# Kernel tuning notes

Hardware: AMD Instinct MI355X
Metric: run time of the kernel (lower is better)

The kernel has to match this reference:

```python
import jax, jax.numpy as jnp
import numpy as np

N_NODES = 300000   # cell instances
N_NETS  = 200000   # hyperedges (nets); each net has exactly one source/driver
E_SINK  = 1000000  # sink (node->net) pin edges
NODE_DIM, NET_DIM, EMB = 32, 16, 64
L, NUM_VN = 3, 1000
OUT_NODE, OUT_NET = 4, 4
SLOPE = 0.01  # torch leaky_relu default negative_slope


def leaky(x):
    return jnp.where(x >= 0, x, SLOPE * x)


def _lin(key, fan_in, fan_out):
    kw, kb = jax.random.split(key)
    b = 1.0 / np.sqrt(fan_in)
    W = jax.random.uniform(kw, (fan_in, fan_out), jnp.float32, -b, b)
    bb = jax.random.uniform(kb, (fan_out,), jnp.float32, -b, b)
    return W, bb


def setup_inputs() -> dict:
    key = jax.random.key(0)
    ks = iter(jax.random.split(key, 64))
    d = {}
    d["node_features"] = jax.random.normal(next(ks), (N_NODES, NODE_DIM), jnp.float32)
    d["net_features"] = jax.random.normal(next(ks), (N_NETS, NET_DIM), jnp.float32)
    d["src_nodes"] = jax.random.randint(next(ks), (N_NETS,), 0, N_NODES)   # driver node of net i
    d["sink_nodes"] = jax.random.randint(next(ks), (E_SINK,), 0, N_NODES)
    d["sink_nets"] = jax.random.randint(next(ks), (E_SINK,), 0, N_NETS)
    d["edge_weight"] = jax.random.uniform(next(ks), (E_SINK,), jnp.float32)
    d["batch"] = jax.random.randint(next(ks), (N_NODES,), 0, NUM_VN)       # node -> virtual node id
    # node / net encoders
    d["ne_W1"], d["ne_b1"] = _lin(next(ks), NODE_DIM, 2 * EMB)
    d["ne_W2"], d["ne_b2"] = _lin(next(ks), 2 * EMB, EMB)
    d["te_W1"], d["te_b1"] = _lin(next(ks), NET_DIM, EMB)
    d["te_W2"], d["te_b2"] = _lin(next(ks), EMB, EMB)
    d["vn_emb"] = jnp.zeros((EMB,), jnp.float32)  # torch: init.constant_(weight, 0)
    # HyperConv layers, stacked over L
    Wnet, bnet, Wnode, bnode = [], [], [], []
    for _ in range(L):
        W, b = _lin(next(ks), 3 * EMB, EMB); Wnet.append(W); bnet.append(b)
        W, b = _lin(next(ks), 2 * EMB, EMB); Wnode.append(W); bnode.append(b)
    d["conv_Wnet"] = jnp.stack(Wnet); d["conv_bnet"] = jnp.stack(bnet)
    d["conv_Wnode"] = jnp.stack(Wnode); d["conv_bnode"] = jnp.stack(bnode)
    # virtual-node MLPs (L-1 of them)
    vW1, vb1, vW2, vb2 = [], [], [], []
    for _ in range(L - 1):
        W, b = _lin(next(ks), EMB, EMB); vW1.append(W); vb1.append(b)
        W, b = _lin(next(ks), EMB, EMB); vW2.append(W); vb2.append(b)
    d["vn_W1"] = jnp.stack(vW1); d["vn_b1"] = jnp.stack(vb1)
    d["vn_W2"] = jnp.stack(vW2); d["vn_b2"] = jnp.stack(vb2)
    # output heads
    d["fc1n_W"], d["fc1n_b"] = _lin(next(ks), EMB, 256)
    d["fc2n_W"], d["fc2n_b"] = _lin(next(ks), 256, OUT_NODE)
    d["fc1e_W"], d["fc1e_b"] = _lin(next(ks), EMB, 64)
    d["fc2e_W"], d["fc2e_b"] = _lin(next(ks), 64, OUT_NET)
    return d


def _forward(node_features, net_features, edge_weight,
             ne_W1, ne_b1, ne_W2, ne_b2, te_W1, te_b1, te_W2, te_b2,
             vn_emb, conv_Wnet, conv_bnet, conv_Wnode, conv_bnode,
             vn_W1, vn_b1, vn_W2, vn_b2,
             fc1n_W, fc1n_b, fc2n_W, fc2n_b, fc1e_W, fc1e_b, fc2e_W, fc2e_b,
             src_nodes, sink_nodes, sink_nets, batch):
    h = leaky(node_features @ ne_W1 + ne_b1) @ ne_W2 + ne_b2   # [N, EMB]
    g = leaky(net_features @ te_W1 + te_b1) @ te_W2 + te_b2    # [M, EMB]
    w = edge_weight[:, None]
    vn = jnp.broadcast_to(vn_emb, (NUM_VN, EMB))               # embedding of all-zero indices
    for l in range(L):
        h = h + vn[batch]
        # node -> net (hyperedge) aggregation: driver message + weighted sink sum
        agg_src = h[src_nodes]                                             # [M, EMB]
        agg_sink = jax.ops.segment_sum(h[sink_nodes] * w, sink_nets, num_segments=N_NETS)
        g = jnp.concatenate([g, agg_src, agg_sink], axis=-1) @ conv_Wnet[l] + conv_bnet[l]
        # net -> node aggregation
        back = jax.ops.segment_sum(g, src_nodes, num_segments=N_NODES) \
             + jax.ops.segment_sum(g[sink_nets] * w, sink_nodes, num_segments=N_NODES)
        h = jnp.concatenate([h, back], axis=-1) @ conv_Wnode[l] + conv_bnode[l]
        h = leaky(h)
        g = leaky(g)
        if l < L - 1:
            pooled = jax.ops.segment_max(h, batch, num_segments=NUM_VN)   # global_max_pool
            tmp = pooled + vn
            vn = vn + (leaky(tmp @ vn_W1[l] + vn_b1[l]) @ vn_W2[l] + vn_b2[l])
    node_rep = jnp.abs(leaky(h @ fc1n_W + fc1n_b) @ fc2n_W + fc2n_b)
    net_rep = jnp.abs(leaky(g @ fc1e_W + fc1e_b) @ fc2e_W + fc2e_b)
    return node_rep, net_rep


def reference(node_features, net_features, edge_weight,
              ne_W1, ne_b1, ne_W2, ne_b2, te_W1, te_b1, te_W2, te_b2,
              vn_emb, conv_Wnet, conv_bnet, conv_Wnode, conv_bnode,
              vn_W1, vn_b1, vn_W2, vn_b2,
              fc1n_W, fc1n_b, fc2n_W, fc2n_b, fc1e_W, fc1e_b, fc2e_W, fc2e_b,
              src_nodes, sink_nodes, sink_nets, batch):
    return _forward(node_features, net_features, edge_weight,
                    ne_W1, ne_b1, ne_W2, ne_b2, te_W1, te_b1, te_W2, te_b2,
                    vn_emb, conv_Wnet, conv_bnet, conv_Wnode, conv_bnode,
                    vn_W1, vn_b1, vn_W2, vn_b2,
                    fc1n_W, fc1n_b, fc2n_W, fc2n_b, fc1e_W, fc1e_b, fc2e_W, fc2e_b,
                    src_nodes, sink_nodes, sink_nets, batch)
```

## Files before the change

kernel.cpp:

```cpp
#include <hip/hip_runtime.h>
#include <cstdint>

static constexpr int N_NODES = 300000;
static constexpr int N_NETS  = 200000;
static constexpr int E_SINK  = 1000000;
static constexpr int NODE_DIM = 32;
static constexpr int NET_DIM  = 16;
static constexpr int EMB = 64;
static constexpr int NUM_VN = 1000;
#define SLOPE 0.01f

typedef __attribute__((ext_vector_type(8))) short bhalf8;
typedef __attribute__((ext_vector_type(4))) float floatx4;
typedef unsigned short u16;

__device__ __forceinline__ float leaky(float x) { return x >= 0.f ? x : SLOPE * x; }

__device__ __forceinline__ unsigned bf16_rne(float x) {
    unsigned u = __float_as_uint(x);
    return (u + 0x7FFFu + ((u >> 16) & 1u)) >> 16;
}
__device__ __forceinline__ void split1(float x, u16& hh, u16& ll) {
    unsigned hb = bf16_rne(x);
    float fh = __uint_as_float(hb << 16);
    unsigned lb = bf16_rne(x - fh);
    hh = (u16)hb; ll = (u16)lb;
}
__device__ __forceinline__ void split8v(const float* x, bhalf8& ah, bhalf8& al) {
#pragma unroll
    for (int e = 0; e < 8; ++e) {
        u16 hh, ll; split1(x[e], hh, ll);
        ah[e] = (short)hh; al[e] = (short)ll;
    }
}
__device__ __forceinline__ float rec1(short h, short l) {
    return __uint_as_float(((unsigned)(u16)h) << 16) +
           __uint_as_float(((unsigned)(u16)l) << 16);
}

__device__ __forceinline__ void afrag_f32(const float* rowp, int kbase, bhalf8& ah, bhalf8& al) {
    float4 v0 = *(const float4*)(rowp + kbase);
    float4 v1 = *(const float4*)(rowp + kbase + 4);
    float x[8] = {v0.x, v0.y, v0.z, v0.w, v1.x, v1.y, v1.z, v1.w};
    split8v(x, ah, al);
}
__device__ __forceinline__ void afrag_hl(const u16* hi, const u16* lo, size_t off,
                                         bhalf8& ah, bhalf8& al) {
    ah = *(const bhalf8*)(hi + off);
    al = *(const bhalf8*)(lo + off);
}

__device__ __forceinline__ floatx4 mm3(bhalf8 ah, bhalf8 al, bhalf8 wh, bhalf8 wl, floatx4 c) {
    c = __builtin_amdgcn_mfma_f32_16x16x32_bf16(ah, wh, c, 0, 0, 0);
    c = __builtin_amdgcn_mfma_f32_16x16x32_bf16(ah, wl, c, 0, 0, 0);
    c = __builtin_amdgcn_mfma_f32_16x16x32_bf16(al, wh, c, 0, 0, 0);
    return c;
}

static constexpr int OFF_NEW1 = 0;
static constexpr int OFF_NEW2 = 4096;
static constexpr int OFF_TEW1 = 12288;
static constexpr int OFF_TEW2 = 14336;
static constexpr int OFF_CWNET = 18432;
static constexpr int OFF_CWNODE = 55296;
static constexpr int OFF_FC1N = 79872;
static constexpr int OFF_FC1E = 96256;
static constexpr int W_TOTAL  = 100352;

__global__ void k_prep_w(const float* __restrict__ neW1, const float* __restrict__ neW2,
                         const float* __restrict__ teW1, const float* __restrict__ teW2,
                         const float* __restrict__ cWnet, const float* __restrict__ cWnode,
                         const float* __restrict__ fc1n, const float* __restrict__ fc1e,
                         u16* __restrict__ wfh, u16* __restrict__ wfl)
{
    int i = blockIdx.x * 256 + threadIdx.x;
    if (i >= W_TOTAL) return;
    int r, ncols, K; const float* src;
    if (i < OFF_NEW2)        { r = i;             src = neW1;  ncols = 128; K = 32; }
    else if (i < OFF_TEW1)   { r = i - OFF_NEW2;  src = neW2;  ncols = 64;  K = 128; }
    else if (i < OFF_TEW2)   { r = i - OFF_TEW1;  src = teW1;  ncols = 64;  K = 16; }
    else if (i < OFF_CWNET)  { r = i - OFF_TEW2;  src = teW2;  ncols = 64;  K = 64; }
    else if (i < OFF_CWNODE) { int t = i - OFF_CWNET;  int l = t / 12288; r = t % 12288;
                               src = cWnet + (size_t)l * 192 * 64; ncols = 64; K = 192; }
    else if (i < OFF_FC1N)   { int t = i - OFF_CWNODE; int l = t / 8192;  r = t % 8192;
                               src = cWnode + (size_t)l * 128 * 64; ncols = 64; K = 128; }
    else if (i < OFF_FC1E)   { r = i - OFF_FC1N;  src = fc1n;  ncols = 256; K = 64; }
    else                     { r = i - OFF_FC1E;  src = fc1e;  ncols = 64;  K = 64; }
    int e = r & 7, g = (r >> 3) & 3;
    int cidx = r >> 5;
    int col = cidx % ncols, kt = cidx / ncols;
    int k = kt * 32 + g * 8 + e;
    float v = (k < K) ? src[(size_t)k * ncols + col] : 0.f;
    u16 hh, ll; split1(v, hh, ll);
    wfh[i] = hh; wfl[i] = ll;
}

__device__ __forceinline__ bhalf8 ldw(const u16* p, int idx) {
    return *(const bhalf8*)(p + idx);
}

__global__ void k_hist_edges(const int* __restrict__ sink_nets, const int* __restrict__ sink_nodes,
                             int* __restrict__ cnt_net, int* __restrict__ cnt_node)
{
    int e = blockIdx.x * 256 + threadIdx.x;
    if (e >= E_SINK) return;
    atomicAdd(&cnt_net[sink_nets[e]], 1);
    atomicAdd(&cnt_node[sink_nodes[e]], 1);
}

__global__ void k_hist_misc(const int* __restrict__ src_nodes, const int* __restrict__ batch,
                            int* __restrict__ cnt_src, int* __restrict__ cnt_vn)
{
    int i = blockIdx.x * 256 + threadIdx.x;
    if (i < N_NETS) atomicAdd(&cnt_src[src_nodes[i]], 1);
    if (i < N_NODES) atomicAdd(&cnt_vn[batch[i]], 1);
}

__global__ void k_scan1(const int* __restrict__ cnt, int n, int* __restrict__ bsum) {
    __shared__ int s[256];
    int i = blockIdx.x * 256 + threadIdx.x;
    s[threadIdx.x] = (i < n) ? cnt[i] : 0;
    __syncthreads();
    for (int off = 128; off; off >>= 1) {
        if (threadIdx.x < off) s[threadIdx.x] += s[threadIdx.x + off];
        __syncthreads();
    }
    if (threadIdx.x == 0) bsum[blockIdx.x] = s[0];
}

__global__ void k_scan2(int* __restrict__ data, int n) {
    __shared__ int s[256];
    __shared__ int carry_s;
    int tid = threadIdx.x;
    if (tid == 0) carry_s = 0;
    __syncthreads();
    for (int base = 0; base < n; base += 256) {
        int i = base + tid;
        int v = (i < n) ? data[i] : 0;
        s[tid] = v;
        __syncthreads();
        for (int off = 1; off < 256; off <<= 1) {
            int t = (tid >= off) ? s[tid - off] : 0;
            __syncthreads();
            s[tid] += t;
            __syncthreads();
        }
        int excl = s[tid] - v + carry_s;
        if (i < n) data[i] = excl;
        __syncthreads();
        if (tid == 255) carry_s = excl + v;
        __syncthreads();
    }
}

__global__ void k_scan3(const int* __restrict__ cnt, int n, const int* __restrict__ bsum,
                        int* __restrict__ start) {
    __shared__ int s[256];
    int i = blockIdx.x * 256 + threadIdx.x;
    int v = (i < n) ? cnt[i] : 0;
    s[threadIdx.x] = v;
    __syncthreads();
    for (int off = 1; off < 256; off <<= 1) {
        int t = (threadIdx.x >= off) ? s[threadIdx.x - off] : 0;
        __syncthreads();
        s[threadIdx.x] += t;
        __syncthreads();
    }
    int excl = s[threadIdx.x] - v + bsum[blockIdx.x];
    if (i < n) start[i] = excl;
    if (i == n - 1) start[n] = excl + v;
}

__global__ void k_fill_edges(const int* __restrict__ sink_nets, const int* __restrict__ sink_nodes,
                             const float* __restrict__ ew,
                             const int* __restrict__ net_start, const int* __restrict__ node_start,
                             int* __restrict__ cur_net, int* __restrict__ cur_node,
                             int* __restrict__ e_node, float* __restrict__ e_w,
                             int* __restrict__ e2_net, float* __restrict__ e2_w)
{
    int e = blockIdx.x * 256 + threadIdx.x;
    if (e >= E_SINK) return;
    int tn = sink_nets[e], dn = sink_nodes[e];
    float w = ew[e];
    int p = net_start[tn] + atomicAdd(&cur_net[tn], 1);
    e_node[p] = dn; e_w[p] = w;
    int q = node_start[dn] + atomicAdd(&cur_node[dn], 1);
    e2_net[q] = tn; e2_w[q] = w;
}

__global__ void k_fill_misc(const int* __restrict__ src_nodes, const int* __restrict__ batch,
                            const int* __restrict__ src_start, const int* __restrict__ vn_start,
                            int* __restrict__ cur_src, int* __restrict__ cur_vn,
                            int* __restrict__ s_net, int* __restrict__ b_node)
{
    int i = blockIdx.x * 256 + threadIdx.x;
    if (i < N_NETS) {
        int d = src_nodes[i];
        int p = src_start[d] + atomicAdd(&cur_src[d], 1);
        s_net[p] = i;
    }
    if (i < N_NODES) {
        int v = batch[i];
        int p = vn_start[v] + atomicAdd(&cur_vn[v], 1);
        b_node[p] = i;
    }
}

__global__ __launch_bounds__(256) void k_gather_agg(
    u16* __restrict__ agg_hi, u16* __restrict__ agg_lo,
    const u16* __restrict__ h_hi, const u16* __restrict__ h_lo,
    const int* __restrict__ net_start, const int* __restrict__ e_node, const float* __restrict__ e_w)
{
    int w = (blockIdx.x * 256 + threadIdx.x) >> 6;
    if (w >= N_NETS) return;
    int lane = threadIdx.x & 63;
    int grp = lane >> 3, l8 = lane & 7;
    int j0 = net_start[w], j1 = net_start[w + 1];
    float a[8] = {0.f, 0.f, 0.f, 0.f, 0.f, 0.f, 0.f, 0.f};
    for (int j = j0 + grp; j < j1; j += 8) {
        int idx = e_node[j];
        float wt = e_w[j];
        size_t off = (size_t)idx * 64 + l8 * 8;
        bhalf8 vh = *(const bhalf8*)(h_hi + off);
        bhalf8 vl = *(const bhalf8*)(h_lo + off);
#pragma unroll
        for (int e = 0; e < 8; ++e) a[e] += wt * rec1(vh[e], vl[e]);
    }
#pragma unroll
    for (int e = 0; e < 8; ++e) {
        a[e] += __shfl_xor(a[e], 8, 64);
        a[e] += __shfl_xor(a[e], 16, 64);
        a[e] += __shfl_xor(a[e], 32, 64);
    }
    if (grp == 0) {
        bhalf8 oh, ol;
        split8v(a, oh, ol);
        size_t off = (size_t)w * 64 + l8 * 8;
        *(bhalf8*)(agg_hi + off) = oh;
        *(bhalf8*)(agg_lo + off) = ol;
    }
}

__global__ __launch_bounds__(256) void k_gather_back(
    u16* __restrict__ back_hi, u16* __restrict__ back_lo,
    const u16* __restrict__ g_hi, const u16* __restrict__ g_lo,
    const int* __restrict__ src_start, const int* __restrict__ s_net,
    const int* __restrict__ node_start, const int* __restrict__ e2_net, const float* __restrict__ e2_w)
{
    int w = (blockIdx.x * 256 + threadIdx.x) >> 6;
    if (w >= N_NODES) return;
    int lane = threadIdx.x & 63;
    int grp = lane >> 3, l8 = lane & 7;
    float a[8] = {0.f, 0.f, 0.f, 0.f, 0.f, 0.f, 0.f, 0.f};
    int j0 = src_start[w], j1 = src_start[w + 1];
    for (int j = j0 + grp; j < j1; j += 8) {
        int idx = s_net[j];
        size_t off = (size_t)idx * 64 + l8 * 8;
        bhalf8 vh = *(const bhalf8*)(g_hi + off);
        bhalf8 vl = *(const bhalf8*)(g_lo + off);
#pragma unroll
        for (int e = 0; e < 8; ++e) {
            float f = rec1(vh[e], vl[e]);
            a[e] += (f >= 0.f) ? f : f * 100.f;
        }
    }
    j0 = node_start[w]; j1 = node_start[w + 1];
    for (int j = j0 + grp; j < j1; j += 8) {
        int idx = e2_net[j];
        float wt = e2_w[j];
        size_t off = (size_t)idx * 64 + l8 * 8;
        bhalf8 vh = *(const bhalf8*)(g_hi + off);
        bhalf8 vl = *(const bhalf8*)(g_lo + off);
#pragma unroll
        for (int e = 0; e < 8; ++e) {
            float f = rec1(vh[e], vl[e]);
            a[e] += wt * ((f >= 0.f) ? f : f * 100.f);
        }
    }
#pragma unroll
    for (int e = 0; e < 8; ++e) {
        a[e] += __shfl_xor(a[e], 8, 64);
        a[e] += __shfl_xor(a[e], 16, 64);
        a[e] += __shfl_xor(a[e], 32, 64);
    }
    if (grp == 0) {
        bhalf8 oh, ol;
        split8v(a, oh, ol);
        size_t off = (size_t)w * 64 + l8 * 8;
        *(bhalf8*)(back_hi + off) = oh;
        *(bhalf8*)(back_lo + off) = ol;
    }
}

__global__ __launch_bounds__(256) void k_pool_gather(
    float* __restrict__ pooled, const u16* __restrict__ h_hi, const u16* __restrict__ h_lo,
    const int* __restrict__ vn_start, const int* __restrict__ b_node)
{
    __shared__ float red[32][64];
    int tid = threadIdx.x;
    int grp = tid >> 3, l8 = tid & 7;
    int v = blockIdx.x;
    int j0 = vn_start[v], j1 = vn_start[v + 1];
    const float NEG = -__builtin_inff();
    float m[8] = {NEG, NEG, NEG, NEG, NEG, NEG, NEG, NEG};
    for (int j = j0 + grp; j < j1; j += 32) {
        int nd = b_node[j];
        size_t off = (size_t)nd * 64 + l8 * 8;
        bhalf8 vh = *(const bhalf8*)(h_hi + off);
        bhalf8 vl = *(const bhalf8*)(h_lo + off);
#pragma unroll
        for (int e = 0; e < 8; ++e) m[e] = fmaxf(m[e], rec1(vh[e], vl[e]));
    }
#pragma unroll
    for (int e = 0; e < 8; ++e) red[grp][l8 * 8 + e] = m[e];
    __syncthreads();
    if (tid < 64) {
        float mm = red[0][tid];
#pragma unroll
        for (int q = 1; q < 32; ++q) mm = fmaxf(mm, red[q][tid]);
        pooled[(size_t)v * 64 + tid] = mm;
    }
}

__global__ __launch_bounds__(256) void k_node_enc(
    const float* __restrict__ x, const u16* __restrict__ wfh, const u16* __restrict__ wfl,
    const float* __restrict__ b1, const float* __restrict__ b2,
    u16* __restrict__ h_hi, u16* __restrict__ h_lo)
{
    __shared__ u16 t_hi[64][136];
    __shared__ u16 t_lo[64][136];
    int lane = threadIdx.x & 63, wid = threadIdx.x >> 6;
    int g16 = lane >> 4, l15 = lane & 15;
    int rbase = blockIdx.x * 64;

    bhalf8 W1H[2], W1L[2];
#pragma unroll
    for (int s = 0; s < 2; ++s) {
        int col = wid * 16 + s * 64 + l15;
        int fo = OFF_NEW1 + (col * 4 + g16) * 8;
        W1H[s] = ldw(wfh, fo); W1L[s] = ldw(wfl, fo);
    }
    bhalf8 W2H[4], W2L[4];
    int cs = wid * 16 + l15;
#pragma unroll
    for (int kt = 0; kt < 4; ++kt) {
        int fo = OFF_NEW2 + ((kt * 64 + cs) * 4 + g16) * 8;
        W2H[kt] = ldw(wfh, fo); W2L[kt] = ldw(wfl, fo);
    }

#pragma unroll
    for (int ms = 0; ms < 4; ++ms) {
        int r = min(rbase + ms * 16 + l15, N_NODES - 1);
        bhalf8 ah, al;
        afrag_f32(x + (size_t)r * NODE_DIM, g16 * 8, ah, al);
#pragma unroll
        for (int s = 0; s < 2; ++s) {
            floatx4 acc = {0.f, 0.f, 0.f, 0.f};
            acc = mm3(ah, al, W1H[s], W1L[s], acc);
            int hc = wid * 16 + s * 64 + l15;
            float bb = b1[hc];
#pragma unroll
            for (int i = 0; i < 4; ++i) {
                u16 hh, ll;
                split1(leaky(acc[i] + bb), hh, ll);
                t_hi[ms * 16 + g16 * 4 + i][hc] = hh;
                t_lo[ms * 16 + g16 * 4 + i][hc] = ll;
            }
        }
    }
    __syncthreads();

    float bias = b2[cs];
#pragma unroll
    for (int ms = 0; ms < 4; ++ms) {
        floatx4 acc = {0.f, 0.f, 0.f, 0.f};
#pragma unroll
        for (int kt = 0; kt < 4; ++kt) {
            bhalf8 ah = *(const bhalf8*)(&t_hi[ms * 16 + l15][kt * 32 + g16 * 8]);
            bhalf8 al = *(const bhalf8*)(&t_lo[ms * 16 + l15][kt * 32 + g16 * 8]);
            acc = mm3(ah, al, W2H[kt], W2L[kt], acc);
        }
#pragma unroll
        for (int i = 0; i < 4; ++i) {
            int r = rbase + ms * 16 + g16 * 4 + i;
            if (r < N_NODES) {
                u16 hh, ll;
                split1(acc[i] + bias, hh, ll);
                h_hi[(size_t)r * 64 + cs] = hh;
                h_lo[(size_t)r * 64 + cs] = ll;
            }
        }
    }
}

__global__ __launch_bounds__(256) void k_net_enc(
    const float* __restrict__ x, const u16* __restrict__ wfh, const u16* __restrict__ wfl,
    const float* __restrict__ b1, const float* __restrict__ b2,
    u16* __restrict__ g_hi, u16* __restrict__ g_lo)
{
    __shared__ u16 t_hi[64][72];
    __shared__ u16 t_lo[64][72];
    int lane = threadIdx.x & 63, wid = threadIdx.x >> 6;
    int g16 = lane >> 4, l15 = lane & 15;
    int rbase = blockIdx.x * 64;
    int cs = wid * 16 + l15;

    int fo = OFF_TEW1 + (cs * 4 + g16) * 8;
    bhalf8 W1H = ldw(wfh, fo), W1L = ldw(wfl, fo);
    bhalf8 W2H[2], W2L[2];
#pragma unroll
    for (int kt = 0; kt < 2; ++kt) {
        int f2 = OFF_TEW2 + ((kt * 64 + cs) * 4 + g16) * 8;
        W2H[kt] = ldw(wfh, f2); W2L[kt] = ldw(wfl, f2);
    }

#pragma unroll
    for (int ms = 0; ms < 4; ++ms) {
        int r = min(rbase + ms * 16 + l15, N_NETS - 1);
        bhalf8 ah = {0,0,0,0,0,0,0,0}, al = {0,0,0,0,0,0,0,0};
        if (g16 < 2) afrag_f32(x + (size_t)r * NET_DIM, g16 * 8, ah, al);
        floatx4 acc = {0.f, 0.f, 0.f, 0.f};
        acc = mm3(ah, al, W1H, W1L, acc);
        float bb = b1[cs];
#pragma unroll
        for (int i = 0; i < 4; ++i) {
            u16 hh, ll;
            split1(leaky(acc[i] + bb), hh, ll);
            t_hi[ms * 16 + g16 * 4 + i][cs] = hh;
            t_lo[ms * 16 + g16 * 4 + i][cs] = ll;
        }
    }
    __syncthreads();

    float bias = b2[cs];
#pragma unroll
    for (int ms = 0; ms < 4; ++ms) {
        floatx4 acc = {0.f, 0.f, 0.f, 0.f};
#pragma unroll
        for (int kt = 0; kt < 2; ++kt) {
            bhalf8 ah = *(const bhalf8*)(&t_hi[ms * 16 + l15][kt * 32 + g16 * 8]);
            bhalf8 al = *(const bhalf8*)(&t_lo[ms * 16 + l15][kt * 32 + g16 * 8]);
            acc = mm3(ah, al, W2H[kt], W2L[kt], acc);
        }
#pragma unroll
        for (int i = 0; i < 4; ++i) {
            int r = rbase + ms * 16 + g16 * 4 + i;
            if (r < N_NETS) {
                u16 hh, ll;
                split1(acc[i] + bias, hh, ll);
                g_hi[(size_t)r * 64 + cs] = hh;
                g_lo[(size_t)r * 64 + cs] = ll;
            }
        }
    }
}

__global__ void k_vn_init(float* __restrict__ vn, const float* __restrict__ vn_emb) {
    int idx = blockIdx.x * blockDim.x + threadIdx.x;
    if (idx < NUM_VN * EMB) vn[idx] = vn_emb[idx & 63];
}

__global__ void k_add_vn(u16* __restrict__ h_hi, u16* __restrict__ h_lo,
                         const float* __restrict__ vn, const int* __restrict__ batch) {
    int idx = blockIdx.x * blockDim.x + threadIdx.x;
    if (idx >= N_NODES * 8) return;
    int n = idx >> 3, c8 = idx & 7;
    size_t off = (size_t)n * 64 + c8 * 8;
    bhalf8 vh = *(const bhalf8*)(h_hi + off);
    bhalf8 vl = *(const bhalf8*)(h_lo + off);
    const float* vr = vn + (size_t)batch[n] * 64 + c8 * 8;
    float out[8];
#pragma unroll
    for (int e = 0; e < 8; ++e) out[e] = rec1(vh[e], vl[e]) + vr[e];
    bhalf8 oh, ol;
    split8v(out, oh, ol);
    *(bhalf8*)(h_hi + off) = oh;
    *(bhalf8*)(h_lo + off) = ol;
}

__global__ __launch_bounds__(256) void k_conv_net(
    u16* g_hi, u16* g_lo,
    const u16* __restrict__ h_hi, const u16* __restrict__ h_lo,
    const u16* __restrict__ s_hi, const u16* __restrict__ s_lo,
    const int* __restrict__ src,
    const u16* __restrict__ wfh, const u16* __restrict__ wfl, int wbase,
    const float* __restrict__ b)
{
    int lane = threadIdx.x & 63, wid = threadIdx.x >> 6;
    int g16 = lane >> 4, l15 = lane & 15;
    int rbase = blockIdx.x * 64;
    int cs = wid * 16 + l15;

    bhalf8 WH[6], WL[6];
#pragma unroll
    for (int kt = 0; kt < 6; ++kt) {
        int fo = wbase + ((kt * 64 + cs) * 4 + g16) * 8;
        WH[kt] = ldw(wfh, fo); WL[kt] = ldw(wfl, fo);
    }

    bhalf8 GH[4][2], GL[4][2];
#pragma unroll
    for (int ms = 0; ms < 4; ++ms) {
        int r = min(rbase + ms * 16 + l15, N_NETS - 1);
#pragma unroll
        for (int kt = 0; kt < 2; ++kt)
            afrag_hl(g_hi, g_lo, (size_t)r * 64 + kt * 32 + g16 * 8, GH[ms][kt], GL[ms][kt]);
    }
    __syncthreads();

    float bias = b[cs];
#pragma unroll
    for (int ms = 0; ms < 4; ++ms) {
        floatx4 acc = {0.f, 0.f, 0.f, 0.f};
#pragma unroll
        for (int kt = 0; kt < 2; ++kt) acc = mm3(GH[ms][kt], GL[ms][kt], WH[kt], WL[kt], acc);
        int ar = min(rbase + ms * 16 + l15, N_NETS - 1);
        size_t srow = (size_t)src[ar] * 64;
#pragma unroll
        for (int kt = 0; kt < 2; ++kt) {
            bhalf8 ah, al;
            afrag_hl(h_hi, h_lo, srow + kt * 32 + g16 * 8, ah, al);
            acc = mm3(ah, al, WH[2 + kt], WL[2 + kt], acc);
        }
#pragma unroll
        for (int kt = 0; kt < 2; ++kt) {
            bhalf8 ah, al;
            afrag_hl(s_hi, s_lo, (size_t)ar * 64 + kt * 32 + g16 * 8, ah, al);
            acc = mm3(ah, al, WH[4 + kt], WL[4 + kt], acc);
        }
#pragma unroll
        for (int i = 0; i < 4; ++i) {
            int r = rbase + ms * 16 + g16 * 4 + i;
            if (r < N_NETS) {
                u16 hh, ll;
                split1(leaky(acc[i] + bias), hh, ll);
                g_hi[(size_t)r * 64 + cs] = hh;
                g_lo[(size_t)r * 64 + cs] = ll;
            }
        }
    }
}

__global__ __launch_bounds__(256) void k_conv_node(
    u16* h_hi, u16* h_lo,
    const u16* __restrict__ s_hi, const u16* __restrict__ s_lo,
    const u16* __restrict__ wfh, const u16* __restrict__ wfl, int wbase,
    const float* __restrict__ b)
{
    int lane = threadIdx.x & 63, wid = threadIdx.x >> 6;
    int g16 = lane >> 4, l15 = lane & 15;
    int rbase = blockIdx.x * 64;
    int cs = wid * 16 + l15;

    bhalf8 WH[4], WL[4];
#pragma unroll
    for (int kt = 0; kt < 4; ++kt) {
        int fo = wbase + ((kt * 64 + cs) * 4 + g16) * 8;
        WH[kt] = ldw(wfh, fo); WL[kt] = ldw(wfl, fo);
    }

    bhalf8 HH[4][2], HL[4][2];
#pragma unroll
    for (int ms = 0; ms < 4; ++ms) {
        int r = min(rbase + ms * 16 + l15, N_NODES - 1);
#pragma unroll
        for (int kt = 0; kt < 2; ++kt)
            afrag_hl(h_hi, h_lo, (size_t)r * 64 + kt * 32 + g16 * 8, HH[ms][kt], HL[ms][kt]);
    }
    __syncthreads();

    float bias = b[cs];
#pragma unroll
    for (int ms = 0; ms < 4; ++ms) {
        floatx4 acc = {0.f, 0.f, 0.f, 0.f};
#pragma unroll
        for (int kt = 0; kt < 2; ++kt) acc = mm3(HH[ms][kt], HL[ms][kt], WH[kt], WL[kt], acc);
        int ar = min(rbase + ms * 16 + l15, N_NODES - 1);
#pragma unroll
        for (int kt = 0; kt < 2; ++kt) {
            bhalf8 ah, al;
            afrag_hl(s_hi, s_lo, (size_t)ar * 64 + kt * 32 + g16 * 8, ah, al);
            acc = mm3(ah, al, WH[2 + kt], WL[2 + kt], acc);
        }
#pragma unroll
        for (int i = 0; i < 4; ++i) {
            int r = rbase + ms * 16 + g16 * 4 + i;
            if (r < N_NODES) {
                u16 hh, ll;
                split1(leaky(acc[i] + bias), hh, ll);
                h_hi[(size_t)r * 64 + cs] = hh;
                h_lo[(size_t)r * 64 + cs] = ll;
            }
        }
    }
}

__global__ __launch_bounds__(256) void k_vn_update(
    float* __restrict__ vn, const float* __restrict__ pooled,
    const float* __restrict__ W1, const float* __restrict__ b1,
    const float* __restrict__ W2, const float* __restrict__ b2)
{
    int wv = threadIdx.x >> 6, lane = threadIdx.x & 63;
    int v = blockIdx.x * 4 + wv;
    if (v >= NUM_VN) return;
    float p = pooled[(size_t)v * 64 + lane];
    float vv = vn[v * 64 + lane];
    float tmp = p + vv;
    float t1 = b1[lane];
#pragma unroll 16
    for (int k = 0; k < 64; ++k) t1 += __shfl(tmp, k, 64) * W1[k * 64 + lane];
    t1 = leaky(t1);
    float t2 = b2[lane];
#pragma unroll 16
    for (int k = 0; k < 64; ++k) t2 += __shfl(t1, k, 64) * W2[k * 64 + lane];
    vn[v * 64 + lane] = vv + t2;
}

__global__ __launch_bounds__(256) void k_fc_node(
    float* __restrict__ out, const u16* __restrict__ h_hi, const u16* __restrict__ h_lo,
    const u16* __restrict__ wfh, const u16* __restrict__ wfl,
    const float* __restrict__ b1, const float* __restrict__ W2, const float* __restrict__ b2)
{
    __shared__ float red[4][64][4];
    int lane = threadIdx.x & 63, wid = threadIdx.x >> 6;
    int g16 = lane >> 4, l15 = lane & 15;
    int rbase = blockIdx.x * 64;

    bhalf8 W1H[4][2], W1L[4][2];
    float4 w2v[4];
    float b1v[4];
#pragma unroll
    for (int s = 0; s < 4; ++s) {
        int hc = wid * 16 + s * 64 + l15;
#pragma unroll
        for (int kt = 0; kt < 2; ++kt) {
            int fo = OFF_FC1N + ((kt * 256 + hc) * 4 + g16) * 8;
            W1H[s][kt] = ldw(wfh, fo); W1L[s][kt] = ldw(wfl, fo);
        }
        w2v[s] = *(const float4*)(W2 + hc * 4);
        b1v[s] = b1[hc];
    }

#pragma unroll
    for (int ms = 0; ms < 4; ++ms) {
        int r = min(rbase + ms * 16 + l15, N_NODES - 1);
        bhalf8 ah[2], al[2];
#pragma unroll
        for (int kt = 0; kt < 2; ++kt)
            afrag_hl(h_hi, h_lo, (size_t)r * 64 + kt * 32 + g16 * 8, ah[kt], al[kt]);
        float po[4][4] = {{0.f,0.f,0.f,0.f},{0.f,0.f,0.f,0.f},{0.f,0.f,0.f,0.f},{0.f,0.f,0.f,0.f}};
#pragma unroll
        for (int s = 0; s < 4; ++s) {
            floatx4 acc = {0.f, 0.f, 0.f, 0.f};
#pragma unroll
            for (int kt = 0; kt < 2; ++kt) acc = mm3(ah[kt], al[kt], W1H[s][kt], W1L[s][kt], acc);
#pragma unroll
            for (int i = 0; i < 4; ++i) {
                float act = leaky(acc[i] + b1v[s]);
                po[i][0] += act * w2v[s].x;
                po[i][1] += act * w2v[s].y;
                po[i][2] += act * w2v[s].z;
                po[i][3] += act * w2v[s].w;
            }
        }
#pragma unroll
        for (int i = 0; i < 4; ++i)
#pragma unroll
            for (int o = 0; o < 4; ++o) {
                po[i][o] += __shfl_xor(po[i][o], 1, 64);
                po[i][o] += __shfl_xor(po[i][o], 2, 64);
                po[i][o] += __shfl_xor(po[i][o], 4, 64);
                po[i][o] += __shfl_xor(po[i][o], 8, 64);
            }
        if (l15 == 0) {
#pragma unroll
            for (int i = 0; i < 4; ++i)
#pragma unroll
                for (int o = 0; o < 4; ++o)
                    red[wid][ms * 16 + g16 * 4 + i][o] = po[i][o];
        }
    }
    __syncthreads();
    int tid = threadIdx.x;
    int row = tid >> 2, o = tid & 3;
    float sum = red[0][row][o] + red[1][row][o] + red[2][row][o] + red[3][row][o];
    int r = rbase + row;
    if (r < N_NODES) out[(size_t)r * 4 + o] = fabsf(sum + b2[o]);
}

__global__ __launch_bounds__(256) void k_fc_net(
    float* __restrict__ out, const u16* __restrict__ g_hi, const u16* __restrict__ g_lo,
    const u16* __restrict__ wfh, const u16* __restrict__ wfl,
    const float* __restrict__ b1, const float* __restrict__ W2, const float* __restrict__ b2)
{
    __shared__ float red[4][64][4];
    int lane = threadIdx.x & 63, wid = threadIdx.x >> 6;
    int g16 = lane >> 4, l15 = lane & 15;
    int rbase = blockIdx.x * 64;
    int cs = wid * 16 + l15;

    bhalf8 W1H[2], W1L[2];
#pragma unroll
    for (int kt = 0; kt < 2; ++kt) {
        int fo = OFF_FC1E + ((kt * 64 + cs) * 4 + g16) * 8;
        W1H[kt] = ldw(wfh, fo); W1L[kt] = ldw(wfl, fo);
    }
    float4 w2v = *(const float4*)(W2 + cs * 4);
    float b1v = b1[cs];

#pragma unroll
    for (int ms = 0; ms < 4; ++ms) {
        int r = min(rbase + ms * 16 + l15, N_NETS - 1);
        bhalf8 ah[2], al[2];
#pragma unroll
        for (int kt = 0; kt < 2; ++kt)
            afrag_hl(g_hi, g_lo, (size_t)r * 64 + kt * 32 + g16 * 8, ah[kt], al[kt]);
        floatx4 acc = {0.f, 0.f, 0.f, 0.f};
#pragma unroll
        for (int kt = 0; kt < 2; ++kt) acc = mm3(ah[kt], al[kt], W1H[kt], W1L[kt], acc);
        float po[4][4];
#pragma unroll
        for (int i = 0; i < 4; ++i) {
            float act = leaky(acc[i] + b1v);
            po[i][0] = act * w2v.x;
            po[i][1] = act * w2v.y;
            po[i][2] = act * w2v.z;
            po[i][3] = act * w2v.w;
        }
#pragma unroll
        for (int i = 0; i < 4; ++i)
#pragma unroll
            for (int o = 0; o < 4; ++o) {
                po[i][o] += __shfl_xor(po[i][o], 1, 64);
                po[i][o] += __shfl_xor(po[i][o], 2, 64);
                po[i][o] += __shfl_xor(po[i][o], 4, 64);
                po[i][o] += __shfl_xor(po[i][o], 8, 64);
            }
        if (l15 == 0) {
#pragma unroll
            for (int i = 0; i < 4; ++i)
#pragma unroll
                for (int o = 0; o < 4; ++o)
                    red[wid][ms * 16 + g16 * 4 + i][o] = po[i][o];
        }
    }
    __syncthreads();
    int tid = threadIdx.x;
    int row = tid >> 2, o = tid & 3;
    float sum = red[0][row][o] + red[1][row][o] + red[2][row][o] + red[3][row][o];
    int r = rbase + row;
    if (r < N_NETS) out[(size_t)r * 4 + o] = fabsf(sum + b2[o]);
}

extern "C" void kernel_launch(void* const* d_in, const int* in_sizes, int n_in,
                              void* d_out, int out_size, void* d_ws, size_t ws_size,
                              hipStream_t stream)
{
    const float* node_features = (const float*)d_in[0];
    const float* net_features  = (const float*)d_in[1];
    const int*   src_nodes     = (const int*)d_in[2];
    const int*   sink_nodes    = (const int*)d_in[3];
    const int*   sink_nets     = (const int*)d_in[4];
    const float* edge_weight   = (const float*)d_in[5];
    const int*   batch         = (const int*)d_in[6];
    const float* ne_W1 = (const float*)d_in[7];
    const float* ne_b1 = (const float*)d_in[8];
    const float* ne_W2 = (const float*)d_in[9];
    const float* ne_b2 = (const float*)d_in[10];
    const float* te_W1 = (const float*)d_in[11];
    const float* te_b1 = (const float*)d_in[12];
    const float* te_W2 = (const float*)d_in[13];
    const float* te_b2 = (const float*)d_in[14];
    const float* vn_emb = (const float*)d_in[15];
    const float* conv_Wnet  = (const float*)d_in[16];
    const float* conv_bnet  = (const float*)d_in[17];
    const float* conv_Wnode = (const float*)d_in[18];
    const float* conv_bnode = (const float*)d_in[19];
    const float* vn_W1 = (const float*)d_in[20];
    const float* vn_b1 = (const float*)d_in[21];
    const float* vn_W2 = (const float*)d_in[22];
    const float* vn_b2 = (const float*)d_in[23];
    const float* fc1n_W = (const float*)d_in[24];
    const float* fc1n_b = (const float*)d_in[25];
    const float* fc2n_W = (const float*)d_in[26];
    const float* fc2n_b = (const float*)d_in[27];
    const float* fc1e_W = (const float*)d_in[28];
    const float* fc1e_b = (const float*)d_in[29];
    const float* fc2e_W = (const float*)d_in[30];
    const float* fc2e_b = (const float*)d_in[31];

    float* out_node = (float*)d_out;
    float* out_net  = out_node + (size_t)N_NODES * 4;

    u16* h_hi = (u16*)d_ws;
    u16* h_lo = h_hi + (size_t)N_NODES * 64;
    u16* g_hi = h_lo + (size_t)N_NODES * 64;
    u16* g_lo = g_hi + (size_t)N_NETS * 64;
    u16* s_hi = g_lo + (size_t)N_NETS * 64;
    u16* s_lo = s_hi + (size_t)N_NODES * 64;
    u16* wfh  = s_lo + (size_t)N_NODES * 64;
    u16* wfl  = wfh + W_TOTAL;
    float* vn     = (float*)(wfl + W_TOTAL);
    float* pooled = vn + (size_t)NUM_VN * EMB;
    int* net_start  = (int*)(pooled + (size_t)NUM_VN * EMB);
    int* node_start = net_start + (N_NETS + 1);
    int* src_start  = node_start + (N_NODES + 1);
    int* vn_start   = src_start + (N_NODES + 1);
    int*   e_node = vn_start + (NUM_VN + 1);
    float* e_w    = (float*)(e_node + E_SINK);
    int*   e2_net = (int*)(e_w + E_SINK);
    float* e2_w   = (float*)(e2_net + E_SINK);
    int*   s_net  = (int*)(e2_w + E_SINK);
    int*   b_node = s_net + N_NETS;
    int*   cnt    = b_node + N_NODES;
    int*   cnt_net  = cnt;
    int*   cnt_node = cnt + N_NETS;
    int*   cnt_src  = cnt_node + N_NODES;
    int*   cnt_vn   = cnt_src + N_NODES;
    const int CNT_TOTAL = N_NETS + N_NODES + N_NODES + NUM_VN;
    int*   bsum   = cnt + CNT_TOTAL;

    const int nodeTiles = (N_NODES + 63) / 64;
    const int netTiles  = (N_NETS + 63) / 64;
    const int vnBlocks  = (NUM_VN + 3) / 4;
    const int vnElemBlocks  = (NUM_VN * EMB + 255) / 256;
    const int addVnBlocks  = (N_NODES * 8 + 255) / 256;
    const int edgeThreadBlocks = (E_SINK + 255) / 256;
    const int miscThreadBlocks = (N_NODES + 255) / 256;
    const int netWaveBlocks  = (N_NETS + 3) / 4;
    const int nodeWaveBlocks = (N_NODES + 3) / 4;
    const int prepBlocks = (W_TOTAL + 255) / 256;

    hipMemsetAsync(cnt, 0, (size_t)CNT_TOTAL * sizeof(int), stream);
    k_hist_edges<<<edgeThreadBlocks, 256, 0, stream>>>(sink_nets, sink_nodes, cnt_net, cnt_node);
    k_hist_misc<<<miscThreadBlocks, 256, 0, stream>>>(src_nodes, batch, cnt_src, cnt_vn);

    auto scan = [&](int* cnt_arr, int n, int* start_arr) {
        int nb = (n + 255) / 256;
        k_scan1<<<nb, 256, 0, stream>>>(cnt_arr, n, bsum);
        k_scan2<<<1, 256, 0, stream>>>(bsum, nb);
        k_scan3<<<nb, 256, 0, stream>>>(cnt_arr, n, bsum, start_arr);
    };
    scan(cnt_net, N_NETS, net_start);
    scan(cnt_node, N_NODES, node_start);
    scan(cnt_src, N_NODES, src_start);
    scan(cnt_vn, NUM_VN, vn_start);

    hipMemsetAsync(cnt, 0, (size_t)CNT_TOTAL * sizeof(int), stream);
    k_fill_edges<<<edgeThreadBlocks, 256, 0, stream>>>(sink_nets, sink_nodes, edge_weight,
        net_start, node_start, cnt_net, cnt_node, e_node, e_w, e2_net, e2_w);
    k_fill_misc<<<miscThreadBlocks, 256, 0, stream>>>(src_nodes, batch, src_start, vn_start,
        cnt_src, cnt_vn, s_net, b_node);

    k_prep_w<<<prepBlocks, 256, 0, stream>>>(ne_W1, ne_W2, te_W1, te_W2,
                                             conv_Wnet, conv_Wnode, fc1n_W, fc1e_W, wfh, wfl);
    k_node_enc<<<nodeTiles, 256, 0, stream>>>(node_features, wfh, wfl, ne_b1, ne_b2, h_hi, h_lo);
    k_net_enc<<<netTiles, 256, 0, stream>>>(net_features, wfh, wfl, te_b1, te_b2, g_hi, g_lo);
    k_vn_init<<<vnElemBlocks, 256, 0, stream>>>(vn, vn_emb);

    for (int l = 0; l < 3; ++l) {
        k_add_vn<<<addVnBlocks, 256, 0, stream>>>(h_hi, h_lo, vn, batch);

        k_gather_agg<<<netWaveBlocks, 256, 0, stream>>>(s_hi, s_lo, h_hi, h_lo,
                                                        net_start, e_node, e_w);
        k_conv_net<<<netTiles, 256, 0, stream>>>(g_hi, g_lo, h_hi, h_lo, s_hi, s_lo, src_nodes,
            wfh, wfl, OFF_CWNET + l * 12288, conv_bnet + (size_t)l * 64);

        k_gather_back<<<nodeWaveBlocks, 256, 0, stream>>>(s_hi, s_lo, g_hi, g_lo,
            src_start, s_net, node_start, e2_net, e2_w);
        k_conv_node<<<nodeTiles, 256, 0, stream>>>(h_hi, h_lo, s_hi, s_lo,
            wfh, wfl, OFF_CWNODE + l * 8192, conv_bnode + (size_t)l * 64);

        if (l < 2) {
            k_pool_gather<<<NUM_VN, 256, 0, stream>>>(pooled, h_hi, h_lo, vn_start, b_node);
            k_vn_update<<<vnBlocks, 256, 0, stream>>>(vn, pooled,
                vn_W1 + (size_t)l * 64 * 64, vn_b1 + (size_t)l * 64,
                vn_W2 + (size_t)l * 64 * 64, vn_b2 + (size_t)l * 64);
        }
    }

    k_fc_node<<<nodeTiles, 256, 0, stream>>>(out_node, h_hi, h_lo, wfh, wfl,
                                             fc1n_b, fc2n_W, fc2n_b);
    k_fc_net<<<netTiles, 256, 0, stream>>>(out_net, g_hi, g_lo, wfh, wfl,
                                           fc1e_b, fc2e_W, fc2e_b);
}
```

Before: 1.792 ms.

## Keep fp32 copies of node/net features for gathers and pack edge index+weight

Adds optional fp32 mirrors of h and of the raw pre-activation g, written by the encoder and conv epilogues, so the sparse gather, back-scatter and pooling kernels read one contiguous fp32 row instead of two bf16 hi/lo arrays and then reconstructing. The back gather reads raw g directly and skips undoing the leaky activation. Edge index and weight are packed into int2 so each edge needs one load instead of two. In exchange the epilogues write extra fp32 data, the fp32 path only runs when the workspace is large enough, and total bytes per gathered row stay the same.

```diff
diff --git a/kernel.cpp b/kernel.cpp
--- a/kernel.cpp
+++ b/kernel.cpp
@@ -175,17 +175,16 @@
                              const float* __restrict__ ew,
                              const int* __restrict__ net_start, const int* __restrict__ node_start,
                              int* __restrict__ cur_net, int* __restrict__ cur_node,
-                             int* __restrict__ e_node, float* __restrict__ e_w,
-                             int* __restrict__ e2_net, float* __restrict__ e2_w)
+                             int2* __restrict__ e_pack, int2* __restrict__ e2_pack)
 {
     int e = blockIdx.x * 256 + threadIdx.x;
     if (e >= E_SINK) return;
     int tn = sink_nets[e], dn = sink_nodes[e];
-    float w = ew[e];
+    int wbits = __float_as_int(ew[e]);
     int p = net_start[tn] + atomicAdd(&cur_net[tn], 1);
-    e_node[p] = dn; e_w[p] = w;
+    e_pack[p] = make_int2(dn, wbits);
     int q = node_start[dn] + atomicAdd(&cur_node[dn], 1);
-    e2_net[q] = tn; e2_w[q] = w;
+    e2_pack[q] = make_int2(tn, wbits);
 }
 
 __global__ void k_fill_misc(const int* __restrict__ src_nodes, const int* __restrict__ batch,
@@ -206,10 +205,11 @@
     }
 }
 
+template<bool HF32>
 __global__ __launch_bounds__(256) void k_gather_agg(
     u16* __restrict__ agg_hi, u16* __restrict__ agg_lo,
-    const u16* __restrict__ h_hi, const u16* __restrict__ h_lo,
-    const int* __restrict__ net_start, const int* __restrict__ e_node, const float* __restrict__ e_w)
+    const u16* __restrict__ h_hi, const u16* __restrict__ h_lo, const float* __restrict__ h_f32,
+    const int* __restrict__ net_start, const int2* __restrict__ e_pack)
 {
     int w = (blockIdx.x * 256 + threadIdx.x) >> 6;
     if (w >= N_NETS) return;
@@ -218,13 +218,20 @@
     int j0 = net_start[w], j1 = net_start[w + 1];
     float a[8] = {0.f, 0.f, 0.f, 0.f, 0.f, 0.f, 0.f, 0.f};
     for (int j = j0 + grp; j < j1; j += 8) {
-        int idx = e_node[j];
-        float wt = e_w[j];
-        size_t off = (size_t)idx * 64 + l8 * 8;
-        bhalf8 vh = *(const bhalf8*)(h_hi + off);
-        bhalf8 vl = *(const bhalf8*)(h_lo + off);
-#pragma unroll
-        for (int e = 0; e < 8; ++e) a[e] += wt * rec1(vh[e], vl[e]);
+        int2 pk = e_pack[j];
+        float wt = __int_as_float(pk.y);
+        if (HF32) {
+            const float4* rp = (const float4*)(h_f32 + (size_t)pk.x * 64 + l8 * 8);
+            float4 v0 = rp[0], v1 = rp[1];
+            a[0] += wt * v0.x; a[1] += wt * v0.y; a[2] += wt * v0.z; a[3] += wt * v0.w;
+            a[4] += wt * v1.x; a[5] += wt * v1.y; a[6] += wt * v1.z; a[7] += wt * v1.w;
+        } else {
+            size_t off = (size_t)pk.x * 64 + l8 * 8;
+            bhalf8 vh = *(const bhalf8*)(h_hi + off);
+            bhalf8 vl = *(const bhalf8*)(h_lo + off);
+#pragma unroll
+            for (int e = 0; e < 8; ++e) a[e] += wt * rec1(vh[e], vl[e]);
+        }
     }
 #pragma unroll
     for (int e = 0; e < 8; ++e) {
@@ -241,11 +248,12 @@
     }
 }
 
+template<bool GF32>
 __global__ __launch_bounds__(256) void k_gather_back(
     u16* __restrict__ back_hi, u16* __restrict__ back_lo,
-    const u16* __restrict__ g_hi, const u16* __restrict__ g_lo,
+    const u16* __restrict__ g_hi, const u16* __restrict__ g_lo, const float* __restrict__ g_raw,
     const int* __restrict__ src_start, const int* __restrict__ s_net,
-    const int* __restrict__ node_start, const int* __restrict__ e2_net, const float* __restrict__ e2_w)
+    const int* __restrict__ node_start, const int2* __restrict__ e2_pack)
 {
     int w = (blockIdx.x * 256 + threadIdx.x) >> 6;
     if (w >= N_NODES) return;
@@ -255,26 +263,40 @@
     int j0 = src_start[w], j1 = src_start[w + 1];
     for (int j = j0 + grp; j < j1; j += 8) {
         int idx = s_net[j];
-        size_t off = (size_t)idx * 64 + l8 * 8;
-        bhalf8 vh = *(const bhalf8*)(g_hi + off);
-        bhalf8 vl = *(const bhalf8*)(g_lo + off);
-#pragma unroll
-        for (int e = 0; e < 8; ++e) {
-            float f = rec1(vh[e], vl[e]);
-            a[e] += (f >= 0.f) ? f : f * 100.f;
+        if (GF32) {
+            const float4* rp = (const float4*)(g_raw + (size_t)idx * 64 + l8 * 8);
+            float4 v0 = rp[0], v1 = rp[1];
+            a[0] += v0.x; a[1] += v0.y; a[2] += v0.z; a[3] += v0.w;
+            a[4] += v1.x; a[5] += v1.y; a[6] += v1.z; a[7] += v1.w;
+        } else {
+            size_t off = (size_t)idx * 64 + l8 * 8;
+            bhalf8 vh = *(const bhalf8*)(g_hi + off);
+            bhalf8 vl = *(const bhalf8*)(g_lo + off);
+#pragma unroll
+            for (int e = 0; e < 8; ++e) {
+                float f = rec1(vh[e], vl[e]);
+                a[e] += (f >= 0.f) ? f : f * 100.f;
+            }
         }
     }
     j0 = node_start[w]; j1 = node_start[w + 1];
     for (int j = j0 + grp; j < j1; j += 8) {
-        int idx = e2_net[j];
-        float wt = e2_w[j];
-        size_t off = (size_t)idx * 64 + l8 * 8;
-        bhalf8 vh = *(const bhalf8*)(g_hi + off);
-        bhalf8 vl = *(const bhalf8*)(g_lo + off);
-#pragma unroll
-        for (int e = 0; e < 8; ++e) {
-            float f = rec1(vh[e], vl[e]);
-            a[e] += wt * ((f >= 0.f) ? f : f * 100.f);
+        int2 pk = e2_pack[j];
+        float wt = __int_as_float(pk.y);
+        if (GF32) {
+            const float4* rp = (const float4*)(g_raw + (size_t)pk.x * 64 + l8 * 8);
+            float4 v0 = rp[0], v1 = rp[1];
+            a[0] += wt * v0.x; a[1] += wt * v0.y; a[2] += wt * v0.z; a[3] += wt * v0.w;
+            a[4] += wt * v1.x; a[5] += wt * v1.y; a[6] += wt * v1.z; a[7] += wt * v1.w;
+        } else {
+            size_t off = (size_t)pk.x * 64 + l8 * 8;
+            bhalf8 vh = *(const bhalf8*)(g_hi + off);
+            bhalf8 vl = *(const bhalf8*)(g_lo + off);
+#pragma unroll
+            for (int e = 0; e < 8; ++e) {
+                float f = rec1(vh[e], vl[e]);
+                a[e] += wt * ((f >= 0.f) ? f : f * 100.f);
+            }
         }
     }
 #pragma unroll
@@ -292,8 +314,10 @@
     }
 }
 
+template<bool HF32>
 __global__ __launch_bounds__(256) void k_pool_gather(
     float* __restrict__ pooled, const u16* __restrict__ h_hi, const u16* __restrict__ h_lo,
+    const float* __restrict__ h_f32,
     const int* __restrict__ vn_start, const int* __restrict__ b_node)
 {
     __shared__ float red[32][64];
@@ -305,11 +329,20 @@
     float m[8] = {NEG, NEG, NEG, NEG, NEG, NEG, NEG, NEG};
     for (int j = j0 + grp; j < j1; j += 32) {
         int nd = b_node[j];
-        size_t off = (size_t)nd * 64 + l8 * 8;
-        bhalf8 vh = *(const bhalf8*)(h_hi + off);
-        bhalf8 vl = *(const bhalf8*)(h_lo + off);
-#pragma unroll
-        for (int e = 0; e < 8; ++e) m[e] = fmaxf(m[e], rec1(vh[e], vl[e]));
+        if (HF32) {
+            const float4* rp = (const float4*)(h_f32 + (size_t)nd * 64 + l8 * 8);
+            float4 v0 = rp[0], v1 = rp[1];
+            m[0] = fmaxf(m[0], v0.x); m[1] = fmaxf(m[1], v0.y);
+            m[2] = fmaxf(m[2], v0.z); m[3] = fmaxf(m[3], v0.w);
+            m[4] = fmaxf(m[4], v1.x); m[5] = fmaxf(m[5], v1.y);
+            m[6] = fmaxf(m[6], v1.z); m[7] = fmaxf(m[7], v1.w);
+        } else {
+            size_t off = (size_t)nd * 64 + l8 * 8;
+            bhalf8 vh = *(const bhalf8*)(h_hi + off);
+            bhalf8 vl = *(const bhalf8*)(h_lo + off);
+#pragma unroll
+            for (int e = 0; e < 8; ++e) m[e] = fmaxf(m[e], rec1(vh[e], vl[e]));
+        }
     }
 #pragma unroll
     for (int e = 0; e < 8; ++e) red[grp][l8 * 8 + e] = m[e];
@@ -325,7 +358,7 @@
 __global__ __launch_bounds__(256) void k_node_enc(
     const float* __restrict__ x, const u16* __restrict__ wfh, const u16* __restrict__ wfl,
     const float* __restrict__ b1, const float* __restrict__ b2,
-    u16* __restrict__ h_hi, u16* __restrict__ h_lo)
+    u16* __restrict__ h_hi, u16* __restrict__ h_lo, float* __restrict__ h_f32)
 {
     __shared__ u16 t_hi[64][136];
     __shared__ u16 t_lo[64][136];
@@ -384,8 +417,10 @@
         for (int i = 0; i < 4; ++i) {
             int r = rbase + ms * 16 + g16 * 4 + i;
             if (r < N_NODES) {
+                float v = acc[i] + bias;
+                if (h_f32) h_f32[(size_t)r * 64 + cs] = v;
                 u16 hh, ll;
-                split1(acc[i] + bias, hh, ll);
+                split1(v, hh, ll);
                 h_hi[(size_t)r * 64 + cs] = hh;
                 h_lo[(size_t)r * 64 + cs] = ll;
             }
@@ -460,18 +495,28 @@
     if (idx < NUM_VN * EMB) vn[idx] = vn_emb[idx & 63];
 }
 
-__global__ void k_add_vn(u16* __restrict__ h_hi, u16* __restrict__ h_lo,
+__global__ void k_add_vn(u16* __restrict__ h_hi, u16* __restrict__ h_lo, float* __restrict__ h_f32,
                          const float* __restrict__ vn, const int* __restrict__ batch) {
     int idx = blockIdx.x * blockDim.x + threadIdx.x;
     if (idx >= N_NODES * 8) return;
     int n = idx >> 3, c8 = idx & 7;
     size_t off = (size_t)n * 64 + c8 * 8;
-    bhalf8 vh = *(const bhalf8*)(h_hi + off);
-    bhalf8 vl = *(const bhalf8*)(h_lo + off);
     const float* vr = vn + (size_t)batch[n] * 64 + c8 * 8;
     float out[8];
-#pragma unroll
-    for (int e = 0; e < 8; ++e) out[e] = rec1(vh[e], vl[e]) + vr[e];
+    if (h_f32) {
+        const float4* hp = (const float4*)(h_f32 + off);
+        float4 v0 = hp[0], v1 = hp[1];
+        out[0] = v0.x + vr[0]; out[1] = v0.y + vr[1]; out[2] = v0.z + vr[2]; out[3] = v0.w + vr[3];
+        out[4] = v1.x + vr[4]; out[5] = v1.y + vr[5]; out[6] = v1.z + vr[6]; out[7] = v1.w + vr[7];
+        float4* wp = (float4*)(h_f32 + off);
+        wp[0] = make_float4(out[0], out[1], out[2], out[3]);
+        wp[1] = make_float4(out[4], out[5], out[6], out[7]);
+    } else {
+        bhalf8 vh = *(const bhalf8*)(h_hi + off);
+        bhalf8 vl = *(const bhalf8*)(h_lo + off);
+#pragma unroll
+        for (int e = 0; e < 8; ++e) out[e] = rec1(vh[e], vl[e]) + vr[e];
+    }
     bhalf8 oh, ol;
     split8v(out, oh, ol);
     *(bhalf8*)(h_hi + off) = oh;
@@ -479,7 +524,7 @@
 }
 
 __global__ __launch_bounds__(256) void k_conv_net(
-    u16* g_hi, u16* g_lo,
+    u16* g_hi, u16* g_lo, float* __restrict__ g_raw,
     const u16* __restrict__ h_hi, const u16* __restrict__ h_lo,
     const u16* __restrict__ s_hi, const u16* __restrict__ s_lo,
     const int* __restrict__ src,
@@ -532,8 +577,10 @@
         for (int i = 0; i < 4; ++i) {
             int r = rbase + ms * 16 + g16 * 4 + i;
             if (r < N_NETS) {
+                float graw = acc[i] + bias;
+                if (g_raw) g_raw[(size_t)r * 64 + cs] = graw;
                 u16 hh, ll;
-                split1(leaky(acc[i] + bias), hh, ll);
+                split1(leaky(graw), hh, ll);
                 g_hi[(size_t)r * 64 + cs] = hh;
                 g_lo[(size_t)r * 64 + cs] = ll;
             }
@@ -542,7 +589,7 @@
 }
 
 __global__ __launch_bounds__(256) void k_conv_node(
-    u16* h_hi, u16* h_lo,
+    u16* h_hi, u16* h_lo, float* __restrict__ h_f32,
     const u16* __restrict__ s_hi, const u16* __restrict__ s_lo,
     const u16* __restrict__ wfh, const u16* __restrict__ wfl, int wbase,
     const float* __restrict__ b)
@@ -586,8 +633,10 @@
         for (int i = 0; i < 4; ++i) {
             int r = rbase + ms * 16 + g16 * 4 + i;
             if (r < N_NODES) {
+                float hval = leaky(acc[i] + bias);
+                if (h_f32) h_f32[(size_t)r * 64 + cs] = hval;
                 u16 hh, ll;
-                split1(leaky(acc[i] + bias), hh, ll);
+                split1(hval, hh, ll);
                 h_hi[(size_t)r * 64 + cs] = hh;
                 h_lo[(size_t)r * 64 + cs] = ll;
             }
@@ -792,33 +841,45 @@
     float* out_node = (float*)d_out;
     float* out_net  = out_node + (size_t)N_NODES * 4;
 
-    u16* h_hi = (u16*)d_ws;
-    u16* h_lo = h_hi + (size_t)N_NODES * 64;
-    u16* g_hi = h_lo + (size_t)N_NODES * 64;
-    u16* g_lo = g_hi + (size_t)N_NETS * 64;
-    u16* s_hi = g_lo + (size_t)N_NETS * 64;
-    u16* s_lo = s_hi + (size_t)N_NODES * 64;
-    u16* wfh  = s_lo + (size_t)N_NODES * 64;
-    u16* wfl  = wfh + W_TOTAL;
-    float* vn     = (float*)(wfl + W_TOTAL);
-    float* pooled = vn + (size_t)NUM_VN * EMB;
-    int* net_start  = (int*)(pooled + (size_t)NUM_VN * EMB);
-    int* node_start = net_start + (N_NETS + 1);
-    int* src_start  = node_start + (N_NODES + 1);
-    int* vn_start   = src_start + (N_NODES + 1);
-    int*   e_node = vn_start + (NUM_VN + 1);
-    float* e_w    = (float*)(e_node + E_SINK);
-    int*   e2_net = (int*)(e_w + E_SINK);
-    float* e2_w   = (float*)(e2_net + E_SINK);
-    int*   s_net  = (int*)(e2_w + E_SINK);
-    int*   b_node = s_net + N_NETS;
-    int*   cnt    = b_node + N_NODES;
-    int*   cnt_net  = cnt;
-    int*   cnt_node = cnt + N_NETS;
-    int*   cnt_src  = cnt_node + N_NODES;
-    int*   cnt_vn   = cnt_src + N_NODES;
+    char* wsp = (char*)d_ws;
+    size_t used = 0;
+    auto alloc = [&](size_t bytes) -> char* {
+        char* r = wsp + used;
+        used += (bytes + 255) & ~(size_t)255;
+        return r;
+    };
+    u16* h_hi = (u16*)alloc((size_t)N_NODES * 64 * 2);
+    u16* h_lo = (u16*)alloc((size_t)N_NODES * 64 * 2);
+    u16* g_hi = (u16*)alloc((size_t)N_NETS * 64 * 2);
+    u16* g_lo = (u16*)alloc((size_t)N_NETS * 64 * 2);
+    u16* s_hi = (u16*)alloc((size_t)N_NODES * 64 * 2);
+    u16* s_lo = (u16*)alloc((size_t)N_NODES * 64 * 2);
+    u16* wfh  = (u16*)alloc((size_t)W_TOTAL * 2);
+    u16* wfl  = (u16*)alloc((size_t)W_TOTAL * 2);
+    float* vn     = (float*)alloc((size_t)NUM_VN * EMB * 4);
+    float* pooled = (float*)alloc((size_t)NUM_VN * EMB * 4);
+    int* net_start  = (int*)alloc((size_t)(N_NETS + 1) * 4);
+    int* node_start = (int*)alloc((size_t)(N_NODES + 1) * 4);
+    int* src_start  = (int*)alloc((size_t)(N_NODES + 1) * 4);
+    int* vn_start   = (int*)alloc((size_t)(NUM_VN + 1) * 4);
+    int2* e_pack  = (int2*)alloc((size_t)E_SINK * 8);
+    int2* e2_pack = (int2*)alloc((size_t)E_SINK * 8);
+    int* s_net  = (int*)alloc((size_t)N_NETS * 4);
+    int* b_node = (int*)alloc((size_t)N_NODES * 4);
     const int CNT_TOTAL = N_NETS + N_NODES + N_NODES + NUM_VN;
-    int*   bsum   = cnt + CNT_TOTAL;
+    int* cnt  = (int*)alloc((size_t)CNT_TOTAL * 4);
+    int* bsum = (int*)alloc(2048 * 4);
+    int* cnt_net  = cnt;
+    int* cnt_node = cnt + N_NETS;
+    int* cnt_src  = cnt_node + N_NODES;
+    int* cnt_vn   = cnt_src + N_NODES;
+
+    float* g_raw = nullptr;
+    if (used + (size_t)N_NETS * 64 * 4 + 256 <= ws_size)
+        g_raw = (float*)alloc((size_t)N_NETS * 64 * 4);
+    float* h_f32 = nullptr;
+    if (used + (size_t)N_NODES * 64 * 4 + 256 <= ws_size)
+        h_f32 = (float*)alloc((size_t)N_NODES * 64 * 4);
 
     const int nodeTiles = (N_NODES + 63) / 64;
     const int netTiles  = (N_NETS + 63) / 64;
@@ -848,31 +909,47 @@
 
     hipMemsetAsync(cnt, 0, (size_t)CNT_TOTAL * sizeof(int), stream);
     k_fill_edges<<<edgeThreadBlocks, 256, 0, stream>>>(sink_nets, sink_nodes, edge_weight,
-        net_start, node_start, cnt_net, cnt_node, e_node, e_w, e2_net, e2_w);
+        net_start, node_start, cnt_net, cnt_node, e_pack, e2_pack);
     k_fill_misc<<<miscThreadBlocks, 256, 0, stream>>>(src_nodes, batch, src_start, vn_start,
         cnt_src, cnt_vn, s_net, b_node);
 
     k_prep_w<<<prepBlocks, 256, 0, stream>>>(ne_W1, ne_W2, te_W1, te_W2,
                                              conv_Wnet, conv_Wnode, fc1n_W, fc1e_W, wfh, wfl);
-    k_node_enc<<<nodeTiles, 256, 0, stream>>>(node_features, wfh, wfl, ne_b1, ne_b2, h_hi, h_lo);
+    k_node_enc<<<nodeTiles, 256, 0, stream>>>(node_features, wfh, wfl, ne_b1, ne_b2,
+                                              h_hi, h_lo, h_f32);
     k_net_enc<<<netTiles, 256, 0, stream>>>(net_features, wfh, wfl, te_b1, te_b2, g_hi, g_lo);
     k_vn_init<<<vnElemBlocks, 256, 0, stream>>>(vn, vn_emb);
 
     for (int l = 0; l < 3; ++l) {
-        k_add_vn<<<addVnBlocks, 256, 0, stream>>>(h_hi, h_lo, vn, batch);
-
-        k_gather_agg<<<netWaveBlocks, 256, 0, stream>>>(s_hi, s_lo, h_hi, h_lo,
-                                                        net_start, e_node, e_w);
-        k_conv_net<<<netTiles, 256, 0, stream>>>(g_hi, g_lo, h_hi, h_lo, s_hi, s_lo, src_nodes,
-            wfh, wfl, OFF_CWNET + l * 12288, conv_bnet + (size_t)l * 64);
-
-        k_gather_back<<<nodeWaveBlocks, 256, 0, stream>>>(s_hi, s_lo, g_hi, g_lo,
-            src_start, s_net, node_start, e2_net, e2_w);
-        k_conv_node<<<nodeTiles, 256, 0, stream>>>(h_hi, h_lo, s_hi, s_lo,
+        k_add_vn<<<addVnBlocks, 256, 0, stream>>>(h_hi, h_lo, h_f32, vn, batch);
+
+        if (h_f32)
+            k_gather_agg<true><<<netWaveBlocks, 256, 0, stream>>>(s_hi, s_lo, h_hi, h_lo, h_f32,
+                                                                  net_start, e_pack);
+        else
+            k_gather_agg<false><<<netWaveBlocks, 256, 0, stream>>>(s_hi, s_lo, h_hi, h_lo, h_f32,
+                                                                   net_start, e_pack);
+
+        k_conv_net<<<netTiles, 256, 0, stream>>>(g_hi, g_lo, g_raw, h_hi, h_lo, s_hi, s_lo,
+            src_nodes, wfh, wfl, OFF_CWNET + l * 12288, conv_bnet + (size_t)l * 64);
+
+        if (g_raw)
+            k_gather_back<true><<<nodeWaveBlocks, 256, 0, stream>>>(s_hi, s_lo, g_hi, g_lo, g_raw,
+                src_start, s_net, node_start, e2_pack);
+        else
+            k_gather_back<false><<<nodeWaveBlocks, 256, 0, stream>>>(s_hi, s_lo, g_hi, g_lo, g_raw,
+                src_start, s_net, node_start, e2_pack);
+
+        k_conv_node<<<nodeTiles, 256, 0, stream>>>(h_hi, h_lo, h_f32, s_hi, s_lo,
             wfh, wfl, OFF_CWNODE + l * 8192, conv_bnode + (size_t)l * 64);
 
         if (l < 2) {
-            k_pool_gather<<<NUM_VN, 256, 0, stream>>>(pooled, h_hi, h_lo, vn_start, b_node);
+            if (h_f32)
+                k_pool_gather<true><<<NUM_VN, 256, 0, stream>>>(pooled, h_hi, h_lo, h_f32,
+                                                                vn_start, b_node);
+            else
+                k_pool_gather<false><<<NUM_VN, 256, 0, stream>>>(pooled, h_hi, h_lo, h_f32,
+                                                                 vn_start, b_node);
             k_vn_update<<<vnBlocks, 256, 0, stream>>>(vn, pooled,
                 vn_W1 + (size_t)l * 64 * 64, vn_b1 + (size_t)l * 64,
                 vn_W2 + (size_t)l * 64 * 64, vn_b2 + (size_t)l * 64);
```

New measurement: 1.779 ms. Within noise of the previous version (-0.7%).
